# Kernel optimization log

Hardware: AMD Instinct MI355X
Metric: run time of the kernel (lower is better)

Reference implementation:

```python
import jax, jax.numpy as jnp
import numpy as np

VOCAB, EMB, HID, B, T = 32000, 256, 256, 64, 2048


def setup_inputs() -> dict:
    key = jax.random.key(0)
    ks = jax.random.split(key, 6)
    s = 1.0 / np.sqrt(HID)
    return {
        "source": jax.random.randint(ks[0], (B, T), 0, VOCAB),
        "embedding": jax.random.normal(ks[1], (VOCAB, EMB), dtype=jnp.float32) * 0.02,
        "W_ih": jax.random.uniform(ks[2], (EMB, HID), jnp.float32, -s, s),
        "W_hh": jax.random.uniform(ks[3], (HID, HID), jnp.float32, -s, s),
        "b_ih": jax.random.uniform(ks[4], (HID,), jnp.float32, -s, s),
        "b_hh": jax.random.uniform(ks[5], (HID,), jnp.float32, -s, s),
    }


def reference(source, embedding, W_ih, W_hh, b_ih, b_hh):
    # embedding lookup: [B, T, EMB]
    embedded = embedding[source]
    # scan over time with carried hidden state (RNNCellManual: tanh cell)
    xs = jnp.swapaxes(embedded, 0, 1)  # [T, B, EMB]

    def step(h, x_t):
        h_new = jnp.tanh(x_t @ W_ih + b_ih + h @ W_hh + b_hh)
        return h_new, None

    h0 = jnp.zeros((source.shape[0], W_hh.shape[0]), dtype=embedding.dtype)
    h_T, _ = jax.lax.scan(step, h0, xs)
    return h_T  # final hidden state [B, HID]
```

## Files before the change

kernel.cpp:

```cpp
#include <hip/hip_runtime.h>

#define TT 2048
#define BB 64
#define HH 256

typedef _Float16 half2_t __attribute__((ext_vector_type(2)));
typedef _Float16 half8_t __attribute__((ext_vector_type(8)));
typedef float f32x4 __attribute__((ext_vector_type(4)));
typedef int i32x4 __attribute__((ext_vector_type(4)));

__global__ void prep_kernel(const float* __restrict__ Wih, const float* __restrict__ Whh,
                            _Float16* __restrict__ WihT, _Float16* __restrict__ WhhT) {
  const int n = blockIdx.x;
  const int k = threadIdx.x;
  WihT[n * HH + k] = (_Float16)Wih[k * HH + n];
  WhhT[n * HH + k] = (_Float16)Whh[k * HH + n];
}

__global__ __launch_bounds__(256, 2) void embed_gemm_kernel(
    const int* __restrict__ source, const float* __restrict__ emb,
    const _Float16* __restrict__ WihT, const float* __restrict__ b_ih,
    const float* __restrict__ b_hh, _Float16* __restrict__ U) {
  const int t = blockIdx.x;
  const int nbase = blockIdx.y * 64;
  __shared__ __align__(16) _Float16 Bs[64][280];

  const int tid = threadIdx.x;
  for (int c = tid; c < 64 * 32; c += 256) {
    const int n = c >> 5;
    const int ko = (c & 31) * 8;
    *(half8_t*)&Bs[n][ko] = *(const half8_t*)(WihT + (size_t)(nbase + n) * HH + ko);
  }
  __syncthreads();

  const int lane = tid & 63;
  const int wave = tid >> 6;
  const int row16 = lane & 15;
  const int quad = lane >> 4;
  const int b = wave * 16 + row16;
  const int src = source[b * TT + t];
  const float* arow = emb + (size_t)src * HH + quad * 8;

  f32x4 acc[4];
#pragma unroll
  for (int ct = 0; ct < 4; ++ct) acc[ct] = (f32x4){0.f, 0.f, 0.f, 0.f};

#pragma unroll
  for (int kt = 0; kt < 8; ++kt) {
    const float4 x0 = *(const float4*)(arow + kt * 32);
    const float4 x1 = *(const float4*)(arow + kt * 32 + 4);
    half8_t af;
    af[0] = (_Float16)x0.x; af[1] = (_Float16)x0.y;
    af[2] = (_Float16)x0.z; af[3] = (_Float16)x0.w;
    af[4] = (_Float16)x1.x; af[5] = (_Float16)x1.y;
    af[6] = (_Float16)x1.z; af[7] = (_Float16)x1.w;
#pragma unroll
    for (int ct = 0; ct < 4; ++ct) {
      const half8_t bf = *(const half8_t*)&Bs[ct * 16 + row16][quad * 8 + kt * 32];
      acc[ct] = __builtin_amdgcn_mfma_f32_16x16x32_f16(af, bf, acc[ct], 0, 0, 0);
    }
  }

#pragma unroll
  for (int ct = 0; ct < 4; ++ct) {
    const int nn = nbase + ct * 16 + row16;
    const float bias = b_ih[nn] + b_hh[nn];
#pragma unroll
    for (int r = 0; r < 4; ++r) {
      const int bb = wave * 16 + quad * 4 + r;
      U[((size_t)t * BB + bb) * HH + nn] = (_Float16)(acc[ct][r] + bias);
    }
  }
}

__global__ __launch_bounds__(256)
__attribute__((amdgpu_waves_per_eu(1, 1)))
void rnn_scan_kernel(
    const _Float16* __restrict__ U, const _Float16* __restrict__ WhhT,
    float* __restrict__ out) {
  const int b = blockIdx.x;
  const int tid = threadIdx.x;
  const int w = tid >> 6;
  const int l = tid & 63;
  const int col = l & 15;
  const int quad = l >> 4;

  __shared__ __align__(16) _Float16 hbuf[2][HH];

  half8_t wb[4][8];
#pragma unroll
  for (int tt = 0; tt < 4; ++tt) {
    const _Float16* base = WhhT + (size_t)(64 * w + 16 * tt + col) * HH + quad * 8;
#pragma unroll
    for (int c = 0; c < 8; ++c) wb[tt][c] = *(const half8_t*)(base + 32 * c);
  }
  asm volatile("" : "+a"(wb[0][0]), "+a"(wb[0][1]), "+a"(wb[0][2]), "+a"(wb[0][3]),
                    "+a"(wb[0][4]), "+a"(wb[0][5]), "+a"(wb[0][6]), "+a"(wb[0][7]),
                    "+a"(wb[1][0]), "+a"(wb[1][1]), "+a"(wb[1][2]), "+a"(wb[1][3]),
                    "+a"(wb[1][4]), "+a"(wb[1][5]), "+a"(wb[1][6]), "+a"(wb[1][7]));
  asm volatile("" : "+a"(wb[2][0]), "+a"(wb[2][1]), "+a"(wb[2][2]), "+a"(wb[2][3]),
                    "+a"(wb[2][4]), "+a"(wb[2][5]), "+a"(wb[2][6]), "+a"(wb[2][7]),
                    "+a"(wb[3][0]), "+a"(wb[3][1]), "+a"(wb[3][2]), "+a"(wb[3][3]),
                    "+a"(wb[3][4]), "+a"(wb[3][5]), "+a"(wb[3][6]), "+a"(wb[3][7]));

  hbuf[0][tid] = (_Float16)0.f;

  const _Float16* Up = U + b * HH + tid;
  _Float16 uc[8], un[8];
#pragma unroll
  for (int s = 0; s < 8; ++s) uc[s] = Up[(size_t)s * (BB * HH)];

  float hn = 0.f;
  __syncthreads();

  for (int tc = 0; tc < TT; tc += 8) {
    const int tn = (tc + 8) & (TT - 1);
#pragma unroll
    for (int s = 0; s < 8; ++s) un[s] = Up[(size_t)(tn + s) * (BB * HH)];

#pragma unroll
    for (int s = 0; s < 8; ++s) {
      const int t = tc + s;

      const _Float16* hrow = hbuf[t & 1] + quad * 8;
      half8_t ha[8];
#pragma unroll
      for (int c = 0; c < 8; ++c) ha[c] = *(const half8_t*)(hrow + 32 * c);
      asm volatile("" : "+v"(ha[0]), "+v"(ha[1]), "+v"(ha[2]), "+v"(ha[3]),
                        "+v"(ha[4]), "+v"(ha[5]), "+v"(ha[6]), "+v"(ha[7]));

      f32x4 cacc[4];
#pragma unroll
      for (int tt = 0; tt < 4; ++tt) cacc[tt] = (f32x4){0.f, 0.f, 0.f, 0.f};
#pragma unroll
      for (int c = 0; c < 8; ++c)
#pragma unroll
        for (int tt = 0; tt < 4; ++tt)
          cacc[tt] = __builtin_amdgcn_mfma_f32_16x16x32_f16(ha[c], wb[tt][c], cacc[tt], 0, 0, 0);

      float y = cacc[0][0];
      y = (quad == 1) ? cacc[1][0] : y;
      y = (quad == 2) ? cacc[2][0] : y;
      y = (quad == 3) ? cacc[3][0] : y;

      const float a = (float)uc[s] + y;
      const float e = __builtin_amdgcn_exp2f(a * 2.885390081777927f);
      hn = 1.f - 2.f * __builtin_amdgcn_rcpf(e + 1.f);
      hbuf[(t + 1) & 1][tid] = (_Float16)hn;

      __syncthreads();
    }
#pragma unroll
    for (int s = 0; s < 8; ++s) uc[s] = un[s];
  }
  out[(size_t)b * HH + tid] = hn;
}

extern "C" void kernel_launch(void* const* d_in, const int* in_sizes, int n_in,
                              void* d_out, int out_size, void* d_ws, size_t ws_size,
                              hipStream_t stream) {
  const int*   source = (const int*)d_in[0];
  const float* emb    = (const float*)d_in[1];
  const float* Wih    = (const float*)d_in[2];
  const float* Whh    = (const float*)d_in[3];
  const float* bih    = (const float*)d_in[4];
  const float* bhh    = (const float*)d_in[5];
  float* out = (float*)d_out;

  char* ws = (char*)d_ws;
  _Float16* U    = (_Float16*)ws;
  _Float16* WihT = (_Float16*)(ws + 67108864);
  _Float16* WhhT = (_Float16*)(ws + 67239936);

  prep_kernel<<<dim3(256), dim3(256), 0, stream>>>(Wih, Whh, WihT, WhhT);
  embed_gemm_kernel<<<dim3(TT, 4), dim3(256), 0, stream>>>(source, emb, WihT, bih, bhh, U);
  rnn_scan_kernel<<<dim3(BB), dim3(256), 0, stream>>>(U, WhhT, out);
}
```

Baseline: 946.6 us.

## Replace scan MFMA matvec with split-K fdot2 and LDS partial reduction

The recurrent matvec in the scan kernel moves from 16x16 MFMA tiles, of which only one row of output was used, to packed-half fdot2 on the vector ALU. Each wave handles a 64-element K slice for four output columns per lane. The four wave partials are written to a double-buffered LDS array and summed after a raw s_barrier. Each wave reads only the slice of h that its own lanes wrote, so a single h buffer and one barrier per step are enough. The aim is to cut per-step latency on the serial recurrence, at the cost of more VALU instructions and an extra LDS round trip.

```diff
diff --git a/kernel.cpp b/kernel.cpp
--- a/kernel.cpp
+++ b/kernel.cpp
@@ -7,7 +7,14 @@
 typedef _Float16 half2_t __attribute__((ext_vector_type(2)));
 typedef _Float16 half8_t __attribute__((ext_vector_type(8)));
 typedef float f32x4 __attribute__((ext_vector_type(4)));
-typedef int i32x4 __attribute__((ext_vector_type(4)));
+
+static __device__ __forceinline__ float fdot2(half2_t a, half2_t b, float c) {
+#if __has_builtin(__builtin_amdgcn_fdot2)
+  return __builtin_amdgcn_fdot2(a, b, c, false);
+#else
+  return c + (float)a[0] * (float)b[0] + (float)a[1] * (float)b[1];
+#endif
+}
 
 __global__ void prep_kernel(const float* __restrict__ Wih, const float* __restrict__ Whh,
                             _Float16* __restrict__ WihT, _Float16* __restrict__ WhhT) {
@@ -82,28 +89,19 @@
   const int tid = threadIdx.x;
   const int w = tid >> 6;
   const int l = tid & 63;
-  const int col = l & 15;
-  const int quad = l >> 4;
 
-  __shared__ __align__(16) _Float16 hbuf[2][HH];
+  __shared__ __align__(16) _Float16 hbuf[HH];
+  __shared__ float pbuf[2][HH][5];
 
-  half8_t wb[4][8];
+  half8_t wreg[4][8];
 #pragma unroll
-  for (int tt = 0; tt < 4; ++tt) {
-    const _Float16* base = WhhT + (size_t)(64 * w + 16 * tt + col) * HH + quad * 8;
+  for (int j = 0; j < 4; ++j) {
+    const _Float16* wp = WhhT + (size_t)(64 * j + l) * HH + 64 * w;
 #pragma unroll
-    for (int c = 0; c < 8; ++c) wb[tt][c] = *(const half8_t*)(base + 32 * c);
+    for (int r = 0; r < 8; ++r) wreg[j][r] = *(const half8_t*)(wp + 8 * r);
   }
-  asm volatile("" : "+a"(wb[0][0]), "+a"(wb[0][1]), "+a"(wb[0][2]), "+a"(wb[0][3]),
-                    "+a"(wb[0][4]), "+a"(wb[0][5]), "+a"(wb[0][6]), "+a"(wb[0][7]),
-                    "+a"(wb[1][0]), "+a"(wb[1][1]), "+a"(wb[1][2]), "+a"(wb[1][3]),
-                    "+a"(wb[1][4]), "+a"(wb[1][5]), "+a"(wb[1][6]), "+a"(wb[1][7]));
-  asm volatile("" : "+a"(wb[2][0]), "+a"(wb[2][1]), "+a"(wb[2][2]), "+a"(wb[2][3]),
-                    "+a"(wb[2][4]), "+a"(wb[2][5]), "+a"(wb[2][6]), "+a"(wb[2][7]),
-                    "+a"(wb[3][0]), "+a"(wb[3][1]), "+a"(wb[3][2]), "+a"(wb[3][3]),
-                    "+a"(wb[3][4]), "+a"(wb[3][5]), "+a"(wb[3][6]), "+a"(wb[3][7]));
 
-  hbuf[0][tid] = (_Float16)0.f;
+  hbuf[tid] = (_Float16)0.f;
 
   const _Float16* Up = U + b * HH + tid;
   _Float16 uc[8], un[8];
@@ -120,35 +118,44 @@
 
 #pragma unroll
     for (int s = 0; s < 8; ++s) {
-      const int t = tc + s;
+      const _Float16* hrow = hbuf + 64 * w;
+      half8_t hv[8];
+#pragma unroll
+      for (int r = 0; r < 8; ++r) hv[r] = *(const half8_t*)(hrow + 8 * r);
 
-      const _Float16* hrow = hbuf[t & 1] + quad * 8;
-      half8_t ha[8];
+      float a0 = 0.f, a1 = 0.f, a2 = 0.f, a3 = 0.f;
 #pragma unroll
-      for (int c = 0; c < 8; ++c) ha[c] = *(const half8_t*)(hrow + 32 * c);
-      asm volatile("" : "+v"(ha[0]), "+v"(ha[1]), "+v"(ha[2]), "+v"(ha[3]),
-                        "+v"(ha[4]), "+v"(ha[5]), "+v"(ha[6]), "+v"(ha[7]));
+      for (int r = 0; r < 8; ++r) {
+#pragma unroll
+        for (int i = 0; i < 4; ++i) {
+          const half2_t hh = {hv[r][2 * i], hv[r][2 * i + 1]};
+          const half2_t w0 = {wreg[0][r][2 * i], wreg[0][r][2 * i + 1]};
+          const half2_t w1 = {wreg[1][r][2 * i], wreg[1][r][2 * i + 1]};
+          const half2_t w2 = {wreg[2][r][2 * i], wreg[2][r][2 * i + 1]};
+          const half2_t w3 = {wreg[3][r][2 * i], wreg[3][r][2 * i + 1]};
+          a0 = fdot2(hh, w0, a0);
+          a1 = fdot2(hh, w1, a1);
+          a2 = fdot2(hh, w2, a2);
+          a3 = fdot2(hh, w3, a3);
+        }
+      }
 
-      f32x4 cacc[4];
-#pragma unroll
-      for (int tt = 0; tt < 4; ++tt) cacc[tt] = (f32x4){0.f, 0.f, 0.f, 0.f};
-#pragma unroll
-      for (int c = 0; c < 8; ++c)
-#pragma unroll
-        for (int tt = 0; tt < 4; ++tt)
-          cacc[tt] = __builtin_amdgcn_mfma_f32_16x16x32_f16(ha[c], wb[tt][c], cacc[tt], 0, 0, 0);
+      pbuf[s & 1][l][w]       = a0;
+      pbuf[s & 1][64 + l][w]  = a1;
+      pbuf[s & 1][128 + l][w] = a2;
+      pbuf[s & 1][192 + l][w] = a3;
 
-      float y = cacc[0][0];
-      y = (quad == 1) ? cacc[1][0] : y;
-      y = (quad == 2) ? cacc[2][0] : y;
-      y = (quad == 3) ? cacc[3][0] : y;
+      asm volatile("s_waitcnt lgkmcnt(0)\n\ts_barrier" ::: "memory");
 
+      const float p0 = pbuf[s & 1][tid][0];
+      const float p1 = pbuf[s & 1][tid][1];
+      const float p2 = pbuf[s & 1][tid][2];
+      const float p3 = pbuf[s & 1][tid][3];
+      const float y = (p0 + p1) + (p2 + p3);
       const float a = (float)uc[s] + y;
       const float e = __builtin_amdgcn_exp2f(a * 2.885390081777927f);
       hn = 1.f - 2.f * __builtin_amdgcn_rcpf(e + 1.f);
-      hbuf[(t + 1) & 1][tid] = (_Float16)hn;
-
-      __syncthreads();
+      hbuf[tid] = (_Float16)hn;
     }
 #pragma unroll
     for (int s = 0; s < 8; ++s) uc[s] = un[s];
```

Result: slower. 1.086 ms (+14.7%).

## Offload one MFMA column tile per wave to VALU dot2 in RNN scan

Applied to the files above, without the earlier changes.

In the serial recurrence, each wave now computes three of its four 16-column output tiles with MFMA and the fourth with VALU fdot2 plus cross-lane shuffle reductions. This shortens the dependent MFMA chain on the critical path by running matrix and vector units in parallel. The per-step __syncthreads is also replaced by a raw lgkmcnt wait and s_barrier. The VALU path adds instructions and shuffles, and the raw barrier drops the vmcnt wait that __syncthreads would include.

```diff
diff --git a/kernel.cpp b/kernel.cpp
--- a/kernel.cpp
+++ b/kernel.cpp
@@ -7,7 +7,14 @@
 typedef _Float16 half2_t __attribute__((ext_vector_type(2)));
 typedef _Float16 half8_t __attribute__((ext_vector_type(8)));
 typedef float f32x4 __attribute__((ext_vector_type(4)));
-typedef int i32x4 __attribute__((ext_vector_type(4)));
+
+static __device__ __forceinline__ float fdot2(half2_t a, half2_t b, float c) {
+#if __has_builtin(__builtin_amdgcn_fdot2)
+  return __builtin_amdgcn_fdot2(a, b, c, false);
+#else
+  return c + (float)a[0] * (float)b[0] + (float)a[1] * (float)b[1];
+#endif
+}
 
 __global__ void prep_kernel(const float* __restrict__ Wih, const float* __restrict__ Whh,
                             _Float16* __restrict__ WihT, _Float16* __restrict__ WhhT) {
@@ -87,9 +94,9 @@
 
   __shared__ __align__(16) _Float16 hbuf[2][HH];
 
-  half8_t wb[4][8];
-#pragma unroll
-  for (int tt = 0; tt < 4; ++tt) {
+  half8_t wb[3][8];
+#pragma unroll
+  for (int tt = 0; tt < 3; ++tt) {
     const _Float16* base = WhhT + (size_t)(64 * w + 16 * tt + col) * HH + quad * 8;
 #pragma unroll
     for (int c = 0; c < 8; ++c) wb[tt][c] = *(const half8_t*)(base + 32 * c);
@@ -99,9 +106,16 @@
                     "+a"(wb[1][0]), "+a"(wb[1][1]), "+a"(wb[1][2]), "+a"(wb[1][3]),
                     "+a"(wb[1][4]), "+a"(wb[1][5]), "+a"(wb[1][6]), "+a"(wb[1][7]));
   asm volatile("" : "+a"(wb[2][0]), "+a"(wb[2][1]), "+a"(wb[2][2]), "+a"(wb[2][3]),
-                    "+a"(wb[2][4]), "+a"(wb[2][5]), "+a"(wb[2][6]), "+a"(wb[2][7]),
-                    "+a"(wb[3][0]), "+a"(wb[3][1]), "+a"(wb[3][2]), "+a"(wb[3][3]),
-                    "+a"(wb[3][4]), "+a"(wb[3][5]), "+a"(wb[3][6]), "+a"(wb[3][7]));
+                    "+a"(wb[2][4]), "+a"(wb[2][5]), "+a"(wb[2][6]), "+a"(wb[2][7]));
+
+  half8_t wd[8];
+  {
+    const _Float16* dbase = WhhT + (size_t)(64 * w + 48 + col) * HH + quad * 8;
+#pragma unroll
+    for (int c = 0; c < 8; ++c) wd[c] = *(const half8_t*)(dbase + 32 * c);
+  }
+  asm volatile("" : "+v"(wd[0]), "+v"(wd[1]), "+v"(wd[2]), "+v"(wd[3]),
+                    "+v"(wd[4]), "+v"(wd[5]), "+v"(wd[6]), "+v"(wd[7]));
 
   hbuf[0][tid] = (_Float16)0.f;
 
@@ -129,26 +143,42 @@
       asm volatile("" : "+v"(ha[0]), "+v"(ha[1]), "+v"(ha[2]), "+v"(ha[3]),
                         "+v"(ha[4]), "+v"(ha[5]), "+v"(ha[6]), "+v"(ha[7]));
 
-      f32x4 cacc[4];
-#pragma unroll
-      for (int tt = 0; tt < 4; ++tt) cacc[tt] = (f32x4){0.f, 0.f, 0.f, 0.f};
+      float d0 = 0.f, d1 = 0.f, d2 = 0.f, d3 = 0.f;
+#pragma unroll
+      for (int c = 0; c < 8; ++c) {
+        const half2_t h0 = {ha[c][0], ha[c][1]}, w0 = {wd[c][0], wd[c][1]};
+        const half2_t h1 = {ha[c][2], ha[c][3]}, w1 = {wd[c][2], wd[c][3]};
+        const half2_t h2 = {ha[c][4], ha[c][5]}, w2 = {wd[c][4], wd[c][5]};
+        const half2_t h3 = {ha[c][6], ha[c][7]}, w3 = {wd[c][6], wd[c][7]};
+        d0 = fdot2(h0, w0, d0);
+        d1 = fdot2(h1, w1, d1);
+        d2 = fdot2(h2, w2, d2);
+        d3 = fdot2(h3, w3, d3);
+      }
+      float dsum = (d0 + d1) + (d2 + d3);
+      dsum += __shfl_xor(dsum, 16, 64);
+      dsum += __shfl_xor(dsum, 32, 64);
+
+      f32x4 cacc[3];
+#pragma unroll
+      for (int tt = 0; tt < 3; ++tt) cacc[tt] = (f32x4){0.f, 0.f, 0.f, 0.f};
 #pragma unroll
       for (int c = 0; c < 8; ++c)
 #pragma unroll
-        for (int tt = 0; tt < 4; ++tt)
+        for (int tt = 0; tt < 3; ++tt)
           cacc[tt] = __builtin_amdgcn_mfma_f32_16x16x32_f16(ha[c], wb[tt][c], cacc[tt], 0, 0, 0);
 
       float y = cacc[0][0];
       y = (quad == 1) ? cacc[1][0] : y;
       y = (quad == 2) ? cacc[2][0] : y;
-      y = (quad == 3) ? cacc[3][0] : y;
+      y = (quad == 3) ? dsum : y;
 
       const float a = (float)uc[s] + y;
       const float e = __builtin_amdgcn_exp2f(a * 2.885390081777927f);
       hn = 1.f - 2.f * __builtin_amdgcn_rcpf(e + 1.f);
       hbuf[(t + 1) & 1][tid] = (_Float16)hn;
 
-      __syncthreads();
+      asm volatile("s_waitcnt lgkmcnt(0)\n\ts_barrier" ::: "memory");
     }
 #pragma unroll
     for (int s = 0; s < 8; ++s) uc[s] = un[s];
```

Measured after the change: 1.220 ms. +28.9%, slower.

## Split recurrent matvec across 8 waves per block in RNN scan

Applied to the files above, without the earlier changes.

The scan kernel now launches 512 threads per batch row, and each of 8 waves owns 32 output columns of W_hh instead of 64. That halves the serial MFMA chain per timestep, from 32 to 16 ops per wave. Only half the lanes write the new hidden state, and __syncthreads is replaced by a raw s_waitcnt plus s_barrier. The cost is a barrier across more waves each step, redundant duplicate lanes, and two waves sharing each SIMD.

```diff
diff --git a/kernel.cpp b/kernel.cpp
--- a/kernel.cpp
+++ b/kernel.cpp
@@ -7,7 +7,6 @@
 typedef _Float16 half2_t __attribute__((ext_vector_type(2)));
 typedef _Float16 half8_t __attribute__((ext_vector_type(8)));
 typedef float f32x4 __attribute__((ext_vector_type(4)));
-typedef int i32x4 __attribute__((ext_vector_type(4)));
 
 __global__ void prep_kernel(const float* __restrict__ Wih, const float* __restrict__ Whh,
                             _Float16* __restrict__ WihT, _Float16* __restrict__ WhhT) {
@@ -73,8 +72,8 @@
   }
 }
 
-__global__ __launch_bounds__(256)
-__attribute__((amdgpu_waves_per_eu(1, 1)))
+__global__ __launch_bounds__(512)
+__attribute__((amdgpu_waves_per_eu(2, 2)))
 void rnn_scan_kernel(
     const _Float16* __restrict__ U, const _Float16* __restrict__ WhhT,
     float* __restrict__ out) {
@@ -87,10 +86,10 @@
 
   __shared__ __align__(16) _Float16 hbuf[2][HH];
 
-  half8_t wb[4][8];
+  half8_t wb[2][8];
 #pragma unroll
-  for (int tt = 0; tt < 4; ++tt) {
-    const _Float16* base = WhhT + (size_t)(64 * w + 16 * tt + col) * HH + quad * 8;
+  for (int tt = 0; tt < 2; ++tt) {
+    const _Float16* base = WhhT + (size_t)(32 * w + 16 * tt + col) * HH + quad * 8;
 #pragma unroll
     for (int c = 0; c < 8; ++c) wb[tt][c] = *(const half8_t*)(base + 32 * c);
   }
@@ -98,14 +97,11 @@
                     "+a"(wb[0][4]), "+a"(wb[0][5]), "+a"(wb[0][6]), "+a"(wb[0][7]),
                     "+a"(wb[1][0]), "+a"(wb[1][1]), "+a"(wb[1][2]), "+a"(wb[1][3]),
                     "+a"(wb[1][4]), "+a"(wb[1][5]), "+a"(wb[1][6]), "+a"(wb[1][7]));
-  asm volatile("" : "+a"(wb[2][0]), "+a"(wb[2][1]), "+a"(wb[2][2]), "+a"(wb[2][3]),
-                    "+a"(wb[2][4]), "+a"(wb[2][5]), "+a"(wb[2][6]), "+a"(wb[2][7]),
-                    "+a"(wb[3][0]), "+a"(wb[3][1]), "+a"(wb[3][2]), "+a"(wb[3][3]),
-                    "+a"(wb[3][4]), "+a"(wb[3][5]), "+a"(wb[3][6]), "+a"(wb[3][7]));
 
-  hbuf[0][tid] = (_Float16)0.f;
+  if (tid < HH) hbuf[0][tid] = (_Float16)0.f;
 
-  const _Float16* Up = U + b * HH + tid;
+  const int nfin = 32 * w + 16 * (quad & 1) + col;
+  const _Float16* Up = U + (size_t)b * HH + nfin;
   _Float16 uc[8], un[8];
 #pragma unroll
   for (int s = 0; s < 8; ++s) uc[s] = Up[(size_t)s * (BB * HH)];
@@ -129,31 +125,27 @@
       asm volatile("" : "+v"(ha[0]), "+v"(ha[1]), "+v"(ha[2]), "+v"(ha[3]),
                         "+v"(ha[4]), "+v"(ha[5]), "+v"(ha[6]), "+v"(ha[7]));
 
-      f32x4 cacc[4];
+      f32x4 cacc[2];
+      cacc[0] = (f32x4){0.f, 0.f, 0.f, 0.f};
+      cacc[1] = (f32x4){0.f, 0.f, 0.f, 0.f};
 #pragma unroll
-      for (int tt = 0; tt < 4; ++tt) cacc[tt] = (f32x4){0.f, 0.f, 0.f, 0.f};
-#pragma unroll
-      for (int c = 0; c < 8; ++c)
-#pragma unroll
-        for (int tt = 0; tt < 4; ++tt)
-          cacc[tt] = __builtin_amdgcn_mfma_f32_16x16x32_f16(ha[c], wb[tt][c], cacc[tt], 0, 0, 0);
+      for (int c = 0; c < 8; ++c) {
+        cacc[0] = __builtin_amdgcn_mfma_f32_16x16x32_f16(ha[c], wb[0][c], cacc[0], 0, 0, 0);
+        cacc[1] = __builtin_amdgcn_mfma_f32_16x16x32_f16(ha[c], wb[1][c], cacc[1], 0, 0, 0);
+      }
 
-      float y = cacc[0][0];
-      y = (quad == 1) ? cacc[1][0] : y;
-      y = (quad == 2) ? cacc[2][0] : y;
-      y = (quad == 3) ? cacc[3][0] : y;
-
+      const float y = (quad & 1) ? cacc[1][0] : cacc[0][0];
       const float a = (float)uc[s] + y;
       const float e = __builtin_amdgcn_exp2f(a * 2.885390081777927f);
       hn = 1.f - 2.f * __builtin_amdgcn_rcpf(e + 1.f);
-      hbuf[(t + 1) & 1][tid] = (_Float16)hn;
+      if (quad < 2) hbuf[(t + 1) & 1][nfin] = (_Float16)hn;
 
-      __syncthreads();
+      asm volatile("s_waitcnt lgkmcnt(0)\n\ts_barrier" ::: "memory");
     }
 #pragma unroll
     for (int s = 0; s < 8; ++s) uc[s] = un[s];
   }
-  out[(size_t)b * HH + tid] = hn;
+  if (quad < 2) out[(size_t)b * HH + nfin] = hn;
 }
 
 extern "C" void kernel_launch(void* const* d_in, const int* in_sizes, int n_in,
@@ -174,5 +166,5 @@
 
   prep_kernel<<<dim3(256), dim3(256), 0, stream>>>(Wih, Whh, WihT, WhhT);
   embed_gemm_kernel<<<dim3(TT, 4), dim3(256), 0, stream>>>(source, emb, WihT, bih, bhh, U);
-  rnn_scan_kernel<<<dim3(BB), dim3(256), 0, stream>>>(U, WhhT, out);
+  rnn_scan_kernel<<<dim3(BB), dim3(512), 0, stream>>>(U, WhhT, out);
 }
```

New measurement: 978.4 us. 3.4% more time.
